# Optimization experiments

Measured on AMD Instinct MI355X. Metric: run time of the kernel, lower is better.

## Reference

```python
import jax, jax.numpy as jnp
import numpy as np

B, N, E, H = 4, 1024, 1024, 16
D = E // H  # head dim = 64
SCALE = float(E) ** 0.5  # NOTE: original scales by embedding_dim**0.5, not head_dim


def setup_inputs() -> dict:
    key = jax.random.key(0)
    ks = jax.random.split(key, 9)
    sd = 1.0 / np.sqrt(E)
    return {
        "q": jax.random.normal(ks[0], (B, N, E), jnp.float32),
        "k": jax.random.normal(ks[1], (B, N, E), jnp.float32),
        "v": jax.random.normal(ks[2], (B, N, E), jnp.float32),
        "Wq": jax.random.normal(ks[3], (E, E), jnp.float32) * sd,
        "bq": jax.random.normal(ks[4], (E,), jnp.float32) * sd,
        "Wk": jax.random.normal(ks[5], (E, E), jnp.float32) * sd,
        "bk": jax.random.normal(ks[6], (E,), jnp.float32) * sd,
        "Wv": jax.random.normal(ks[7], (E, E), jnp.float32) * sd,
        "bv": jax.random.normal(ks[8], (E,), jnp.float32) * sd,
    }


def _split_heads(x):
    # (b, n, h*d) -> (b, h, n, d)
    b, n, _ = x.shape
    return x.reshape(b, n, H, D).transpose(0, 2, 1, 3)


def reference(q, k, v, Wq, bq, Wk, bk, Wv, bv):
    q = _split_heads(q @ Wq.T + bq)
    k = _split_heads(k @ Wk.T + bk)
    v = _split_heads(v @ Wv.T + bv)
    # full NxN scores, scaled by embedding_dim**0.5 (as in original)
    attn = jnp.einsum('bhnd,bhld->bhnl', q, k) / SCALE
    attn = jax.nn.softmax(attn, axis=-1)
    # dropout omitted (eval mode)
    # faithful to original non-standard einsum: sums attn over l, broadcasts v
    out = jnp.einsum('bhnl,bhnd->bhnd', attn, v)
    return (out, attn)
```

## Files before the change

kernel.cpp:

```cpp
#include <hip/hip_runtime.h>
#include <hip/hip_bf16.h>
#include <math.h>

#define Bc 4
#define Nc 1024
#define Ec 1024
#define Hc 16
#define Dc 64
#define Mc 4096
#define OUT0_ELEMS 4194304
#define ATTN_ELEMS 67108864ULL
#define SCRATCH_OFF 58720256

typedef __attribute__((ext_vector_type(4))) float f32x4;
typedef __attribute__((ext_vector_type(16))) float f32x16;
typedef __attribute__((ext_vector_type(8))) short s16x8;

__device__ __forceinline__ short f2bf(float f) {
    union { __bf16 h; short s; } c; c.h = (__bf16)f; return c.s;
}

typedef const __attribute__((address_space(1))) char gch;
typedef __attribute__((address_space(3))) char lch;
__device__ __forceinline__ void gload16(const short* g, short* l) {
    __builtin_amdgcn_global_load_lds((gch*)g, (lch*)l, 16, 0, 0);
}

__global__ __launch_bounds__(256)
void cvt_kernel(const float* __restrict__ xq, const float* __restrict__ xk,
                const float* __restrict__ xv, const float* __restrict__ wq,
                const float* __restrict__ wk, const float* __restrict__ wv,
                short* __restrict__ dst)
{
    const int which = blockIdx.y;
    const float* src; size_t n, off;
    switch (which) {
      case 0:  src = xq; n = 4194304; off = 0;        break;
      case 1:  src = xk; n = 4194304; off = 4194304;  break;
      case 2:  src = xv; n = 4194304; off = 8388608;  break;
      case 3:  src = wq; n = 1048576; off = 12582912; break;
      case 4:  src = wk; n = 1048576; off = 13631488; break;
      default: src = wv; n = 1048576; off = 14680064; break;
    }
    const size_t i = ((size_t)blockIdx.x * 256 + threadIdx.x) * 8;
    if (i >= n) return;
    f32x4 a = *(const f32x4*)(src + i);
    f32x4 b = *(const f32x4*)(src + i + 4);
    s16x8 o;
    o[0] = f2bf(a[0]); o[1] = f2bf(a[1]); o[2] = f2bf(a[2]); o[3] = f2bf(a[3]);
    o[4] = f2bf(b[0]); o[5] = f2bf(b[1]); o[6] = f2bf(b[2]); o[7] = f2bf(b[3]);
    *(s16x8*)(dst + off + i) = o;
}

__global__ __launch_bounds__(256)
void proj_kernel(const short* __restrict__ xall, const short* __restrict__ wall,
                 const float* __restrict__ bq, const float* __restrict__ bk,
                 const float* __restrict__ bv,
                 short* __restrict__ qws, short* __restrict__ kws,
                 float* __restrict__ vout)
{
    const int sel = blockIdx.z;
    const short* X = xall + (size_t)sel * 4194304;
    const short* W = wall + (size_t)sel * 1048576;
    const float* bias = (sel == 0) ? bq : (sel == 1) ? bk : bv;

    __shared__ __align__(16) short lA[2][128 * 32];
    __shared__ __align__(16) short lB[2][128 * 32];

    const int t    = threadIdx.x;
    const int lane = t & 63;
    const int w    = t >> 6;
    const int wr   = w >> 1, wc = w & 1;
    const int li   = lane & 15, g = lane >> 4;
    const int bm   = blockIdx.x * 128;
    const int bn   = blockIdx.y * 128;

    const int sr = lane >> 2;
    const int sc = (lane & 3) * 8;
    const short* Xs = X + (size_t)(bm + w * 32) * Ec + sc;
    const short* Ws = W + (size_t)(bn + w * 32) * Ec + sc;

    f32x4 acc[4][4];
#pragma unroll
    for (int i = 0; i < 4; ++i)
#pragma unroll
        for (int j = 0; j < 4; ++j)
            acc[i][j] = (f32x4){0.f, 0.f, 0.f, 0.f};

#define STAGE(buf, kt)                                                        \
    {                                                                         \
        const int kb = (kt) * 32;                                             \
        _Pragma("unroll")                                                     \
        for (int j = 0; j < 2; ++j) {                                         \
            gload16(Xs + (size_t)(j * 16 + sr) * Ec + kb,                     \
                    &lA[buf][(w * 32 + j * 16) * 32]);                        \
            gload16(Ws + (size_t)(j * 16 + sr) * Ec + kb,                     \
                    &lB[buf][(w * 32 + j * 16) * 32]);                        \
        }                                                                     \
    }

    STAGE(0, 0);
    __syncthreads();

    for (int kt = 0; kt < 32; ++kt) {
        const int cur = kt & 1;
        if (kt < 31) STAGE(cur ^ 1, kt + 1);

        s16x8 aF[4], bF[4];
#pragma unroll
        for (int mt = 0; mt < 4; ++mt)
            aF[mt] = *(const s16x8*)&lA[cur][(wr * 64 + mt * 16 + li) * 32 + g * 8];
#pragma unroll
        for (int nt = 0; nt < 4; ++nt)
            bF[nt] = *(const s16x8*)&lB[cur][(wc * 64 + nt * 16 + li) * 32 + g * 8];
#pragma unroll
        for (int mt = 0; mt < 4; ++mt)
#pragma unroll
            for (int nt = 0; nt < 4; ++nt)
                acc[mt][nt] = __builtin_amdgcn_mfma_f32_16x16x32_bf16(
                    aF[mt], bF[nt], acc[mt][nt], 0, 0, 0);

        __syncthreads();
    }
#undef STAGE

    short* dstBF = (sel == 0) ? qws : kws;
#pragma unroll
    for (int nt = 0; nt < 4; ++nt) {
        const int col = bn + wc * 64 + nt * 16 + li;
        const float bcol = bias[col];
        const int h = col >> 6, d = col & 63;
#pragma unroll
        for (int mt = 0; mt < 4; ++mt) {
#pragma unroll
            for (int r = 0; r < 4; ++r) {
                const int row = bm + wr * 64 + mt * 16 + g * 4 + r;
                const int bb = row >> 10, n = row & 1023;
                const size_t off = ((size_t)(bb * Hc + h) * Nc + n) * Dc + d;
                const float val = acc[mt][nt][r] + bcol;
                if (sel == 2)
                    vout[off] = val;
                else
                    dstBF[off] = f2bf(val);
            }
        }
    }
}

__global__ __launch_bounds__(256, 2)
void attn_kernel(const short* __restrict__ qws, const short* __restrict__ kws,
                 float* __restrict__ attnOut)
{
    const int bid = blockIdx.x;
    const int rb  = (bid >> 3) & 31;
    const int bh  = ((bid & 7) << 3) | (bid >> 8);
    const int t  = threadIdx.x;
    const int w  = t >> 6;
    const int lane = t & 63;
    const int li = lane & 31;
    const int hi = lane >> 5;

    const short* Qb = qws + (size_t)bh * (Nc * Dc);
    const short* Kb = kws + (size_t)bh * (Nc * Dc);

    s16x8 qF[4];
    {
        const short* qp = Qb + (size_t)(rb * 32 + li) * Dc + hi * 8;
#pragma unroll
        for (int s = 0; s < 4; ++s)
            qF[s] = *(const s16x8*)(qp + s * 16);
    }

    f32x16 acc[8];
#pragma unroll
    for (int i = 0; i < 8; ++i) acc[i] = (f32x16)(0.f);

    const int colbase = w * 256;
#pragma unroll
    for (int ct = 0; ct < 8; ++ct) {
        const short* kp = Kb + (size_t)(colbase + ct * 32 + li) * Dc + hi * 8;
#pragma unroll
        for (int s = 0; s < 4; ++s) {
            s16x8 kf = *(const s16x8*)(kp + s * 16);
            acc[ct] = __builtin_amdgcn_mfma_f32_32x32x16_bf16(qF[s], kf, acc[ct], 0, 0, 0);
        }
    }

    float mx[16];
#pragma unroll
    for (int r = 0; r < 16; ++r) {
        float m = acc[0][r];
#pragma unroll
        for (int ct = 1; ct < 8; ++ct) m = fmaxf(m, acc[ct][r]);
#pragma unroll
        for (int off = 1; off < 32; off <<= 1)
            m = fmaxf(m, __shfl_xor(m, off));
        mx[r] = m;
    }

    __shared__ float red[4][32];
    if (li == 0) {
#pragma unroll
        for (int r = 0; r < 16; ++r)
            red[w][(r & 3) + 8 * (r >> 2) + 4 * hi] = mx[r];
    }
    __syncthreads();
    const float c = 1.44269504f / 32.0f;
#pragma unroll
    for (int r = 0; r < 16; ++r) {
        const int row = (r & 3) + 8 * (r >> 2) + 4 * hi;
        float m = fmaxf(fmaxf(red[0][row], red[1][row]),
                        fmaxf(red[2][row], red[3][row]));
        mx[r] = -m * c;
    }
    __syncthreads();

    float sm[16];
#pragma unroll
    for (int r = 0; r < 16; ++r) sm[r] = 0.f;
#pragma unroll
    for (int ct = 0; ct < 8; ++ct) {
#pragma unroll
        for (int r = 0; r < 16; ++r) {
            float p = __builtin_amdgcn_exp2f(fmaf(acc[ct][r], c, mx[r]));
            acc[ct][r] = p;
            sm[r] += p;
        }
    }
#pragma unroll
    for (int r = 0; r < 16; ++r) {
#pragma unroll
        for (int off = 1; off < 32; off <<= 1)
            sm[r] += __shfl_xor(sm[r], off);
    }
    if (li == 0) {
#pragma unroll
        for (int r = 0; r < 16; ++r)
            red[w][(r & 3) + 8 * (r >> 2) + 4 * hi] = sm[r];
    }
    __syncthreads();
#pragma unroll
    for (int r = 0; r < 16; ++r) {
        const int row = (r & 3) + 8 * (r >> 2) + 4 * hi;
        sm[r] = 1.0f / (red[0][row] + red[1][row] + red[2][row] + red[3][row]);
    }

    float* outp = attnOut + (size_t)bh * (Nc * Nc) + (size_t)(rb * 32) * Nc;
#pragma unroll
    for (int ct = 0; ct < 8; ++ct) {
        const int col = colbase + ct * 32 + li;
#pragma unroll
        for (int r = 0; r < 16; ++r) {
            const int row = (r & 3) + 8 * (r >> 2) + 4 * hi;
            __builtin_nontemporal_store(acc[ct][r] * sm[r],
                                        &outp[(size_t)row * Nc + col]);
        }
    }
}

extern "C" void kernel_launch(void* const* d_in, const int* in_sizes, int n_in,
                              void* d_out, int out_size, void* d_ws, size_t ws_size,
                              hipStream_t stream) {
    const float* q  = (const float*)d_in[0];
    const float* k  = (const float*)d_in[1];
    const float* v  = (const float*)d_in[2];
    const float* Wq = (const float*)d_in[3];
    const float* bq = (const float*)d_in[4];
    const float* Wk = (const float*)d_in[5];
    const float* bk = (const float*)d_in[6];
    const float* Wv = (const float*)d_in[7];
    const float* bv = (const float*)d_in[8];

    float* out0 = (float*)d_out;
    float* attn = (float*)d_out + OUT0_ELEMS;

    short* s16  = (short*)(attn + SCRATCH_OFF);
    short* xall = s16;
    short* wall = s16 + 12582912;

    short* qws = (short*)d_ws;
    short* kws = qws + (size_t)Mc * Ec;

    cvt_kernel<<<dim3(2048, 6), 256, 0, stream>>>(q, k, v, Wq, Wk, Wv, s16);
    proj_kernel<<<dim3(32, 8, 3), 256, 0, stream>>>(
        xall, wall, bq, bk, bv, qws, kws, out0);
    attn_kernel<<<2048, 256, 0, stream>>>(qws, kws, attn);
}
```

Measured before the change: 143.1 us.

## Triple-buffer projection GEMM loads and XOR-swizzle LDS layout

Changes the projection GEMM from a double-buffered to a triple-buffered LDS pipeline, prefetching two k-tiles ahead. Each iteration now waits with a partial vmcnt instead of a full syncthreads drain. It also XOR-swizzles the 16-byte column groups in global-to-LDS loads and the matching fragment reads, to cut LDS bank conflicts. The cost is 50% more LDS per block, which may lower occupancy, plus hand-written waitcnt logic that must match the number of outstanding loads.

Result: no change. 140.8 us (-1.6%).

```diff
diff --git a/kernel.cpp b/kernel.cpp
--- a/kernel.cpp
+++ b/kernel.cpp
@@ -11,6 +11,7 @@
 #define OUT0_ELEMS 4194304
 #define ATTN_ELEMS 67108864ULL
 #define SCRATCH_OFF 58720256
+#define NTK 32
 
 typedef __attribute__((ext_vector_type(4))) float f32x4;
 typedef __attribute__((ext_vector_type(16))) float f32x16;
@@ -64,8 +65,8 @@
     const short* W = wall + (size_t)sel * 1048576;
     const float* bias = (sel == 0) ? bq : (sel == 1) ? bk : bv;
 
-    __shared__ __align__(16) short lA[2][128 * 32];
-    __shared__ __align__(16) short lB[2][128 * 32];
+    __shared__ __align__(16) short lA[3][128 * 32];
+    __shared__ __align__(16) short lB[3][128 * 32];
 
     const int t    = threadIdx.x;
     const int lane = t & 63;
@@ -76,9 +77,7 @@
     const int bn   = blockIdx.y * 128;
 
     const int sr = lane >> 2;
-    const int sc = (lane & 3) * 8;
-    const short* Xs = X + (size_t)(bm + w * 32) * Ec + sc;
-    const short* Ws = W + (size_t)(bn + w * 32) * Ec + sc;
+    const int c_ = lane & 3;
 
     f32x4 acc[4][4];
 #pragma unroll
@@ -92,27 +91,35 @@
         const int kb = (kt) * 32;                                             \
         _Pragma("unroll")                                                     \
         for (int j = 0; j < 2; ++j) {                                         \
-            gload16(Xs + (size_t)(j * 16 + sr) * Ec + kb,                     \
+            const int row = w * 32 + j * 16 + sr;                             \
+            const int cg  = (c_ ^ ((row >> 1) & 3)) * 8;                      \
+            gload16(X + (size_t)(bm + row) * Ec + kb + cg,                    \
                     &lA[buf][(w * 32 + j * 16) * 32]);                        \
-            gload16(Ws + (size_t)(j * 16 + sr) * Ec + kb,                     \
+            gload16(W + (size_t)(bn + row) * Ec + kb + cg,                    \
                     &lB[buf][(w * 32 + j * 16) * 32]);                        \
         }                                                                     \
     }
 
     STAGE(0, 0);
-    __syncthreads();
-
-    for (int kt = 0; kt < 32; ++kt) {
-        const int cur = kt & 1;
-        if (kt < 31) STAGE(cur ^ 1, kt + 1);
+    STAGE(1, 1);
+    asm volatile("s_waitcnt vmcnt(4)" ::: "memory");
+    __builtin_amdgcn_s_barrier();
+
+    for (int kt = 0; kt < NTK; ++kt) {
+        const int cur = kt % 3;
+        if (kt + 2 < NTK) STAGE((kt + 2) % 3, kt + 2);
 
         s16x8 aF[4], bF[4];
 #pragma unroll
-        for (int mt = 0; mt < 4; ++mt)
-            aF[mt] = *(const s16x8*)&lA[cur][(wr * 64 + mt * 16 + li) * 32 + g * 8];
-#pragma unroll
-        for (int nt = 0; nt < 4; ++nt)
-            bF[nt] = *(const s16x8*)&lB[cur][(wc * 64 + nt * 16 + li) * 32 + g * 8];
+        for (int mt = 0; mt < 4; ++mt) {
+            const int r = wr * 64 + mt * 16 + li;
+            aF[mt] = *(const s16x8*)&lA[cur][r * 32 + ((g ^ ((r >> 1) & 3)) * 8)];
+        }
+#pragma unroll
+        for (int nt = 0; nt < 4; ++nt) {
+            const int r = wc * 64 + nt * 16 + li;
+            bF[nt] = *(const s16x8*)&lB[cur][r * 32 + ((g ^ ((r >> 1) & 3)) * 8)];
+        }
 #pragma unroll
         for (int mt = 0; mt < 4; ++mt)
 #pragma unroll
@@ -120,7 +127,12 @@
                 acc[mt][nt] = __builtin_amdgcn_mfma_f32_16x16x32_bf16(
                     aF[mt], bF[nt], acc[mt][nt], 0, 0, 0);
 
-        __syncthreads();
+        if (kt + 2 < NTK) {
+            asm volatile("s_waitcnt vmcnt(4)" ::: "memory");
+        } else {
+            asm volatile("s_waitcnt vmcnt(0)" ::: "memory");
+        }
+        __builtin_amdgcn_s_barrier();
     }
 #undef STAGE
 
```
